# Kernel tuning notes

Measured on AMD Instinct MI355X. Metric: run time of the kernel, lower is better.

The kernel has to match this reference:

```python
import jax, jax.numpy as jnp
import numpy as np

D_MODEL = 1024
N_HEADS = 16
N_KV = 4
HEAD_DIM = D_MODEL // N_HEADS  # 64
SEQ = 2048
BATCH = 2
CAP = 50.0
EPS = 1e-5
THETA = 10000.0


def setup_inputs() -> dict:
    key = jax.random.key(0)
    ks = jax.random.split(key, 5)
    s = 0.02  # keep pre-attention logits in a sane range
    return {
        'x':   jax.random.normal(ks[0], (BATCH, SEQ, D_MODEL), dtype=jnp.float32),
        'w_q': jax.random.normal(ks[1], (D_MODEL, N_HEADS * HEAD_DIM), dtype=jnp.float32) * s,
        'w_k': jax.random.normal(ks[2], (D_MODEL, N_KV * HEAD_DIM), dtype=jnp.float32) * s,
        'w_v': jax.random.normal(ks[3], (D_MODEL, N_KV * HEAD_DIM), dtype=jnp.float32) * s,
        'w_o': jax.random.normal(ks[4], (N_HEADS * HEAD_DIM, D_MODEL), dtype=jnp.float32) * s,
    }


def _rms_norm(x, eps=EPS):
    return x * jax.lax.rsqrt(jnp.mean(jnp.square(x), axis=-1, keepdims=True) + eps)


def _rope_cos_sin(seq_len, head_dim, theta=THETA):
    inv_freq = 1.0 / (theta ** (jnp.arange(0, head_dim, 2, dtype=jnp.float32) / head_dim))
    freqs = jnp.arange(seq_len, dtype=jnp.float32)[:, None] * inv_freq[None, :]  # (S, d/2)
    return jnp.cos(freqs)[None, :, None, :], jnp.sin(freqs)[None, :, None, :]  # (1,S,1,d/2)


def _apply_rope(x, cos, sin):
    d = x.shape[-1] // 2
    x1, x2 = x[..., :d], x[..., d:]
    return jnp.concatenate([x1 * cos - x2 * sin, x2 * cos + x1 * sin], axis=-1).astype(x.dtype)


def reference(x, w_q, w_k, w_v, w_o):
    B, S, _ = x.shape
    q = (x @ w_q).reshape(B, S, N_HEADS, HEAD_DIM)
    k = (x @ w_k).reshape(B, S, N_KV, HEAD_DIM)
    v = (x @ w_v).reshape(B, S, N_KV, HEAD_DIM)

    # QK RMS-norm (no learned scale)
    q = _rms_norm(q)
    k = _rms_norm(k)

    cos, sin = _rope_cos_sin(S, HEAD_DIM)
    q = _apply_rope(q, cos, sin)
    k = _apply_rope(k, cos, sin)

    # GQA: repeat kv heads to match query heads
    rep = N_HEADS // N_KV
    k = jnp.repeat(k, rep, axis=2)
    v = jnp.repeat(v, rep, axis=2)

    scores = jnp.einsum('bqhd,bkhd->bhqk', q, k) / np.sqrt(HEAD_DIM).astype(np.float32)
    # softcap in float32, as in the original
    scores = jnp.tanh(scores.astype(jnp.float32) / CAP) * CAP
    causal = jnp.tril(jnp.ones((S, S), dtype=bool))  # (S, S)
    scores = jnp.where(causal[None, None], scores, -jnp.inf)
    probs = jax.nn.softmax(scores, axis=-1)  # dropout=0.0 -> identity

    y = jnp.einsum('bhqk,bkhd->bqhd', probs, v).reshape(B, S, N_HEADS * HEAD_DIM)
    return y @ w_o
```

## Files before the change

kernel.cpp:

```cpp
#include <hip/hip_runtime.h>
#include <hip/hip_bf16.h>
#include <math.h>

#define D_MODEL 1024
#define N_HEADS 16
#define N_KV 4
#define HEAD_DIM 64
#define SEQ 2048
#define BATCH 2
#define M_TOK (BATCH * SEQ)

typedef unsigned int u32;
typedef unsigned short u16;
typedef __attribute__((ext_vector_type(8))) short short8;
typedef __attribute__((ext_vector_type(4))) float f32x4;
typedef __attribute__((ext_vector_type(16))) float f32x16;
typedef __attribute__((ext_vector_type(2))) float f32x2;

#define AS1 __attribute__((address_space(1)))
#define AS3 __attribute__((address_space(3)))

__device__ __forceinline__ u16 f2bf(float f) {
  union { __hip_bfloat16 h; u16 u; } c; c.h = __float2bfloat16(f); return c.u;
}
__device__ __forceinline__ float bf2f(u16 v) {
  union { u32 u; float f; } c; c.u = (u32)v << 16; return c.f;
}
__device__ __forceinline__ u32 cvtpk(float lo, float hi) {
  u32 r; asm("v_cvt_pk_bf16_f32 %0, %1, %2" : "=v"(r) : "v"(lo), "v"(hi)); return r;
}
__device__ __forceinline__ void plswap(u32& a, u32& b) {
  asm volatile("v_permlane32_swap_b32 %0, %1" : "+v"(a), "+v"(b));
}
__device__ __forceinline__ float exp2fast(float x) { return __builtin_amdgcn_exp2f(x); }
__device__ __forceinline__ float rcpfast(float x) { return __builtin_amdgcn_rcpf(x); }
__device__ __forceinline__ f32x2 pk_mul(f32x2 a, f32x2 b) {
  f32x2 d; asm("v_pk_mul_f32 %0, %1, %2" : "=v"(d) : "v"(a), "v"(b)); return d;
}
__device__ __forceinline__ f32x2 pk_fma(f32x2 a, f32x2 b, f32x2 c) {
  f32x2 d; asm("v_pk_fma_f32 %0, %1, %2, %3" : "=v"(d) : "v"(a), "v"(b), "v"(c)); return d;
}

__global__ __launch_bounds__(256) void prep_kernel(const float* __restrict__ x,
                                                   const float* __restrict__ wq,
                                                   const float* __restrict__ wk,
                                                   const float* __restrict__ wv,
                                                   const float* __restrict__ wo,
                                                   u16* __restrict__ xb,
                                                   u16* __restrict__ wT,
                                                   u16* __restrict__ woT) {
  int bx = blockIdx.x;
  if (bx < 512) {
    const size_t base = (size_t)bx * 8192;
#pragma unroll
    for (int j = 0; j < 4; ++j) {
      size_t e = base + j * 2048 + threadIdx.x * 8;
      float4 f0 = *(const float4*)(x + e);
      float4 f1 = *(const float4*)(x + e + 4);
      uint4 u;
      u.x = cvtpk(f0.x, f0.y); u.y = cvtpk(f0.z, f0.w);
      u.z = cvtpk(f1.x, f1.y); u.w = cvtpk(f1.z, f1.w);
      *(uint4*)(xb + e) = u;
    }
    return;
  }
  bx -= 512;
  __shared__ float t[32][33];
  const float* src; u16* dst; int N, ntm, nts;
  if (bx < 1024)      { src = wq; dst = wT;                 N = 1024; ntm = 31; nts = 5; }
  else if (bx < 1280) { bx -= 1024; src = wk; dst = wT + (1024 << 10); N = 256; ntm = 7; nts = 3; }
  else if (bx < 1536) { bx -= 1280; src = wv; dst = wT + (1280 << 10); N = 256; ntm = 7; nts = 3; }
  else                { bx -= 1536; src = wo; dst = woT;    N = 1024; ntm = 31; nts = 5; }
  const int n0 = (bx & ntm) << 5, k0 = (bx >> nts) << 5;
  const int xx = threadIdx.x & 31, y = threadIdx.x >> 5;
#pragma unroll
  for (int i = 0; i < 4; ++i) {
    int r = y + (i << 3);
    t[r][xx] = src[(size_t)(k0 + r) * N + n0 + xx];
  }
  __syncthreads();
#pragma unroll
  for (int i = 0; i < 4; ++i) {
    int r = y + (i << 3);
    dst[(size_t)(n0 + r) * 1024 + k0 + xx] = f2bf(t[xx][r]);
  }
}

__global__ __launch_bounds__(256, 2) void qkvgemm_kernel(const u16* __restrict__ xb,
                                                         const u16* __restrict__ wT,
                                                         u16* __restrict__ Qbf,
                                                         u16* __restrict__ Kbf,
                                                         u16* __restrict__ Vt) {
  __shared__ uint4 SM[4][512];
  const int tid = threadIdx.x;
  const int w = tid >> 6, l = tid & 63;
  const int wr = w >> 1, wc = w & 1;
  int wg = ((int)blockIdx.x & 7) * 48 + ((int)blockIdx.x >> 3);
  const int mt = wg / 12, nb = wg - mt * 12;
  const int m0 = mt << 7;

  f32x4 acc[4][4];
#pragma unroll
  for (int m = 0; m < 4; ++m)
#pragma unroll
    for (int n = 0; n < 4; ++n)
#pragma unroll
      for (int j = 0; j < 4; ++j) acc[m][n][j] = 0.f;

  auto stage = [&](int buf, int k0) {
    const u16* Ab = xb + (size_t)m0 * 1024 + k0;
#pragma unroll
    for (int r = 0; r < 2; ++r) {
      int i = (w << 1) + r;
      int row = (i << 4) + (l >> 2);
      const u16* g = Ab + (size_t)row * 1024 + ((l & 3) << 3);
      __builtin_amdgcn_global_load_lds((const AS1 void*)g,
          (AS3 void*)((char*)SM + (buf << 13) + (i << 10)), 16, 0, 0);
    }
    const u16* Bb = wT + (size_t)(nb << 7) * 1024 + k0;
#pragma unroll
    for (int r = 0; r < 2; ++r) {
      int i = (w << 1) + r;
      int row = (i << 4) + (l >> 2);
      const u16* g = Bb + (size_t)row * 1024 + ((l & 3) << 3);
      __builtin_amdgcn_global_load_lds((const AS1 void*)g,
          (AS3 void*)((char*)SM + ((2 + buf) << 13) + (i << 10)), 16, 0, 0);
    }
  };

  stage(0, 0);
#pragma unroll 1
  for (int kt = 0; kt < 32; ++kt) {
    __syncthreads();
    if (kt + 1 < 32) stage((kt + 1) & 1, (kt + 1) << 5);
    const char* Ab = (const char*)SM + ((kt & 1) << 13);
    const char* Bb = (const char*)SM + ((2 + (kt & 1)) << 13);
    short8 af[4], bf[4];
#pragma unroll
    for (int m = 0; m < 4; ++m)
      af[m] = *(const short8*)(Ab + ((wr * 64 + m * 16 + (l & 15)) << 6) + ((l >> 4) << 4));
#pragma unroll
    for (int n = 0; n < 4; ++n)
      bf[n] = *(const short8*)(Bb + ((wc * 64 + n * 16 + (l & 15)) << 6) + ((l >> 4) << 4));
#pragma unroll
    for (int m = 0; m < 4; ++m)
#pragma unroll
      for (int n = 0; n < 4; ++n)
        acc[m][n] = __builtin_amdgcn_mfma_f32_16x16x32_bf16(af[m], bf[n], acc[m][n], 0, 0, 0);
  }

  __syncthreads();
  const int b = m0 >> 11;
  const int pos0 = (m0 & 2047) + wr * 64;
  const int lg = l >> 4, lc = l & 15;
  u16* lds = (u16*)((char*)SM + (w << 13));

  if (nb < 10) {
    float rs[4][4];
#pragma unroll
    for (int m = 0; m < 4; ++m)
#pragma unroll
      for (int j = 0; j < 4; ++j) {
        float ssq = 0.f;
#pragma unroll
        for (int n = 0; n < 4; ++n) ssq = fmaf(acc[m][n][j], acc[m][n][j], ssq);
        ssq += __shfl_xor(ssq, 1); ssq += __shfl_xor(ssq, 2);
        ssq += __shfl_xor(ssq, 4); ssq += __shfl_xor(ssq, 8);
        rs[m][j] = rsqrtf(ssq * (1.f / 64.f) + 1e-5f);
      }
    const float osc = (nb < 8) ? 0.0025f : 1.0f;
    const float invf0 = powf(10000.0f, (float)lc * (-1.f / 32.f));
    const float invf1 = powf(10000.0f, (float)(lc + 16) * (-1.f / 32.f));
#pragma unroll
    for (int m = 0; m < 4; ++m) {
#pragma unroll
      for (int j = 0; j < 4; ++j) {
        const int row = m * 16 + lg * 4 + j;
        const float pos = (float)(pos0 + row);
        float s0, c0, s1, c1;
        sincosf(pos * invf0, &s0, &c0);
        sincosf(pos * invf1, &s1, &c1);
        const float r_ = rs[m][j];
        float x0 = acc[m][0][j] * r_, x1 = acc[m][1][j] * r_;
        float x2 = acc[m][2][j] * r_, x3 = acc[m][3][j] * r_;
        u16 o0 = f2bf((x0 * c0 - x2 * s0) * osc);
        u16 o1 = f2bf((x1 * c1 - x3 * s1) * osc);
        u16 o2 = f2bf((x2 * c0 + x0 * s0) * osc);
        u16 o3 = f2bf((x3 * c1 + x1 * s1) * osc);
        const int rb = row << 6, xr = (row & 7) << 3;
        lds[rb + (lc ^ xr)] = o0;
        lds[rb + ((16 + lc) ^ xr)] = o1;
        lds[rb + ((32 + lc) ^ xr)] = o2;
        lds[rb + ((48 + lc) ^ xr)] = o3;
      }
    }
  } else {
#pragma unroll
    for (int m = 0; m < 4; ++m)
#pragma unroll
      for (int n = 0; n < 4; ++n) {
        const int d = n * 16 + lc;
        const int tok = m * 16 + lg * 4;
        uint2 u;
        u.x = cvtpk(acc[m][n][0], acc[m][n][1]);
        u.y = cvtpk(acc[m][n][2], acc[m][n][3]);
        *(uint2*)(lds + (d << 6) + (tok ^ ((d & 7) << 3))) = u;
      }
  }
  __syncthreads();

  u16* gp; int rstride;
  if (nb < 8)       { gp = Qbf + ((size_t)((b * 16 + nb * 2 + wc) * 2048 + pos0) << 6); rstride = 64; }
  else if (nb < 10) { gp = Kbf + ((size_t)((b * 4 + (nb - 8) * 2 + wc) * 2048 + pos0) << 6); rstride = 64; }
  else              { gp = Vt + (((size_t)((b * 4 + (nb - 10) * 2 + wc) * 64)) << 11) + pos0; rstride = 2048; }
#pragma unroll
  for (int ic = 0; ic < 8; ++ic) {
    const int c = (ic << 6) + l;
    const int row = c >> 3, col8 = (c & 7) << 3;
    uint4 v = *(const uint4*)(lds + (row << 6) + (col8 ^ ((row & 7) << 3)));
    *(uint4*)(gp + (size_t)row * rstride + col8) = v;
  }
}

__global__ __launch_bounds__(256, 2) void gemm_kernel(const u16* __restrict__ A,
                                                      const u16* __restrict__ BT,
                                                      float* __restrict__ C) {
  __shared__ uint4 SM[4][512];
  const int tid = threadIdx.x;
  const int w = tid >> 6, l = tid & 63;
  const int wr = w >> 1, wc = w & 1;
  int wg = ((int)blockIdx.x & 7) * 32 + ((int)blockIdx.x >> 3);
  const int m0 = (wg >> 3) << 7, n0 = (wg & 7) << 7;

  f32x4 acc[4][4];
#pragma unroll
  for (int m = 0; m < 4; ++m)
#pragma unroll
    for (int n = 0; n < 4; ++n)
#pragma unroll
      for (int j = 0; j < 4; ++j) acc[m][n][j] = 0.f;

  auto stage = [&](int buf, int k0) {
    const u16* Ab = A + (size_t)m0 * 1024 + k0;
#pragma unroll
    for (int r = 0; r < 2; ++r) {
      int i = (w << 1) + r;
      int row = (i << 4) + (l >> 2);
      const u16* g = Ab + (size_t)row * 1024 + ((l & 3) << 3);
      __builtin_amdgcn_global_load_lds((const AS1 void*)g,
          (AS3 void*)((char*)SM + (buf << 13) + (i << 10)), 16, 0, 0);
    }
    const u16* Bb = BT + (size_t)n0 * 1024 + k0;
#pragma unroll
    for (int r = 0; r < 2; ++r) {
      int i = (w << 1) + r;
      int row = (i << 4) + (l >> 2);
      const u16* g = Bb + (size_t)row * 1024 + ((l & 3) << 3);
      __builtin_amdgcn_global_load_lds((const AS1 void*)g,
          (AS3 void*)((char*)SM + ((2 + buf) << 13) + (i << 10)), 16, 0, 0);
    }
  };

  stage(0, 0);
#pragma unroll 1
  for (int kt = 0; kt < 32; ++kt) {
    __syncthreads();
    if (kt + 1 < 32) stage((kt + 1) & 1, (kt + 1) << 5);
    const char* Ab = (const char*)SM + ((kt & 1) << 13);
    const char* Bb = (const char*)SM + ((2 + (kt & 1)) << 13);
    short8 af[4], bf[4];
#pragma unroll
    for (int m = 0; m < 4; ++m)
      af[m] = *(const short8*)(Ab + ((wr * 64 + m * 16 + (l & 15)) << 6) + ((l >> 4) << 4));
#pragma unroll
    for (int n = 0; n < 4; ++n)
      bf[n] = *(const short8*)(Bb + ((wc * 64 + n * 16 + (l & 15)) << 6) + ((l >> 4) << 4));
#pragma unroll
    for (int m = 0; m < 4; ++m)
#pragma unroll
      for (int n = 0; n < 4; ++n)
        acc[m][n] = __builtin_amdgcn_mfma_f32_16x16x32_bf16(af[m], bf[n], acc[m][n], 0, 0, 0);
  }

#pragma unroll
  for (int m = 0; m < 4; ++m) {
    int row0 = m0 + wr * 64 + m * 16 + ((l >> 4) << 2);
#pragma unroll
    for (int n = 0; n < 4; ++n) {
      int col = n0 + wc * 64 + n * 16 + (l & 15);
#pragma unroll
      for (int j = 0; j < 4; ++j)
        C[(size_t)(row0 + j) * 1024 + col] = acc[m][n][j];
    }
  }
}

__global__ __launch_bounds__(256) void combine_kernel(const u16* __restrict__ P0,
                                                      const u16* __restrict__ P1,
                                                      const float* __restrict__ L0,
                                                      const float* __restrict__ L1,
                                                      u16* __restrict__ ybf) {
  const int hrow = (blockIdx.x << 1) + (threadIdx.x >> 7);
  const int chunk = threadIdx.x & 127;
  const int h = chunk >> 3;
  const int b = hrow >> 10, posl = hrow & 1023;
  const size_t tok = (size_t)(b * 2048 + 1024 + posl);
  const float rl = rcpfast(L0[hrow * 16 + h] + L1[hrow * 16 + h]);
  uint4 a = *(const uint4*)(P0 + ((size_t)hrow << 10) + (chunk << 3));
  uint4 c = *(const uint4*)(P1 + ((size_t)hrow << 10) + (chunk << 3));
  uint4 o;
#pragma unroll
  for (int e = 0; e < 4; ++e) {
    u32 ua = ((const u32*)&a)[e], uc = ((const u32*)&c)[e];
    float v0 = (bf2f((u16)(ua & 0xffff)) + bf2f((u16)(uc & 0xffff))) * rl;
    float v1 = (bf2f((u16)(ua >> 16)) + bf2f((u16)(uc >> 16))) * rl;
    ((u32*)&o)[e] = cvtpk(v0, v1);
  }
  *(uint4*)(ybf + tok * 1024 + (chunk << 3)) = o;
}

__device__ __forceinline__ short8 rdfrag(const uint4* lds, int row, int cb) {
  int byte = ((row << 7) + cb) ^ ((row & 7) << 4);
  return *(const short8*)((const char*)lds + byte);
}

__global__ __launch_bounds__(256, 3) void attn_kernel(const u16* __restrict__ Qbf,
                                                      const u16* __restrict__ Kbf,
                                                      const u16* __restrict__ Vt,
                                                      u16* __restrict__ ybf,
                                                      u16* __restrict__ P0,
                                                      u16* __restrict__ P1,
                                                      float* __restrict__ L0,
                                                      float* __restrict__ L1) {
  __shared__ uint4 KV[4][512];
  const int tid = threadIdx.x;
  const int g = blockIdx.x & 7;
  const int u = blockIdx.x >> 3;
  int j, kt0, kt1; bool diagEnd;
  if (u < 32)      { j = u;       kt0 = 0;  kt1 = (j >> 1) + 1; diagEnd = true; }
  else if (u < 64) { j = u;       kt0 = 0;  kt1 = 16;           diagEnd = false; }
  else             { j = 127 - u; kt0 = 16; kt1 = (j >> 1) + 1; diagEnd = true; }
  const bool slot1 = (u >= 64);

  const int b = g >> 2, hkv = g & 3;
  const int w = tid >> 6, l = tid & 63;
  const int ql = l & 31, myh = l >> 5;
  const int h = hkv * 4 + w;
  const int q0 = j << 5;
  const int qg = q0 + ql;

  const u16* Kg = Kbf + (((size_t)g) << 11) * 64;
  const u16* Vg = Vt + (((size_t)g) << 6) * 2048;

  short8 bq[4];
  {
    const u16* Qg = Qbf + ((size_t)((b * 16 + h) * 2048 + qg)) * 64 + myh * 8;
    bq[0] = *(const short8*)(Qg);
    bq[1] = *(const short8*)(Qg + 16);
    bq[2] = *(const short8*)(Qg + 32);
    bq[3] = *(const short8*)(Qg + 48);
  }

  f32x16 o0, o1;
#pragma unroll
  for (int i = 0; i < 16; ++i) { o0[i] = 0.f; o1[i] = 0.f; }
  float l_run = 0.f;

  auto stage = [&](int buf, int kt) {
    const u16* gk = Kg + ((size_t)(kt << 6)) * 64;
    const u16* gv = Vg + (kt << 6);
#pragma unroll
    for (int i = 0; i < 2; ++i) {
      int c = tid + (i << 8);
      int row = c >> 3, off = c & 7;
      uint4 kk4 = *(const uint4*)(gk + row * 64 + (off << 3));
      uint4 vv4 = *(const uint4*)(gv + (size_t)row * 2048 + (off << 3));
      int byte = ((row << 7) + (off << 4)) ^ ((row & 7) << 4);
      *(uint4*)((char*)KV[buf << 1] + byte) = kk4;
      *(uint4*)((char*)KV[(buf << 1) + 1] + byte) = vv4;
    }
  };

  stage(0, kt0);

  const float PC2 = -0.33333333f;
  const float SC1 = 72.13475204444817f;
  const float SC0 = -11.541560327111708f;
  const f32x2 PC2v = {PC2, PC2};
  const f32x2 SC1v = {SC1, SC1};
  const f32x2 SC0v = {SC0, SC0};
  const f32x2 ONEv = {1.0f, 1.0f};

#pragma unroll 1
  for (int kt = kt0; kt < kt1; ++kt) {
    const int buf = kt & 1;
    __syncthreads();
    if (kt + 1 < kt1) stage(buf ^ 1, kt + 1);
    const bool last = diagEnd && (kt == kt1 - 1);
    const bool havehi = !last || (j & 1);
    const uint4* Kl = KV[buf << 1];
    const uint4* Vl = KV[(buf << 1) + 1];

    f32x16 s0, s1;
#pragma unroll
    for (int i = 0; i < 16; ++i) { s0[i] = 0.f; s1[i] = 0.f; }
    __builtin_amdgcn_s_setprio(1);
#pragma unroll
    for (int c = 0; c < 4; ++c) {
      short8 ak = rdfrag(Kl, ql, (c << 5) + (myh << 4));
      s0 = __builtin_amdgcn_mfma_f32_32x32x16_bf16(ak, bq[c], s0, 0, 0, 0);
    }
    if (havehi) {
#pragma unroll
      for (int c = 0; c < 4; ++c) {
        short8 ak = rdfrag(Kl, 32 + ql, (c << 5) + (myh << 4));
        s1 = __builtin_amdgcn_mfma_f32_32x32x16_bf16(ak, bq[c], s1, 0, 0, 0);
      }
    }
    __builtin_amdgcn_s_setprio(0);

    float lsum = 0.f;
    auto cap_full = [&](f32x16& s) {
#pragma unroll
      for (int p = 0; p < 8; ++p) {
        f32x2 z; z.x = s[2 * p]; z.y = s[2 * p + 1];
        f32x2 z2 = pk_mul(z, z);
        f32x2 zc = pk_fma(z2, PC2v, ONEv);
        f32x2 zs = pk_mul(z, SC1v);
        f32x2 ar = pk_fma(zs, zc, SC0v);
        float p0 = exp2fast(ar.x);
        float p1 = exp2fast(ar.y);
        s[2 * p] = p0; s[2 * p + 1] = p1;
        lsum += p0; lsum += p1;
      }
    };
    auto cap_diag = [&](f32x16& s) {
#pragma unroll
      for (int i = 0; i < 16; ++i) {
        int kl = (i & 3) + ((i >> 2) << 3) + (myh << 2);
        float z = s[i];
        float zc = fmaf(z * z, PC2, 1.0f);
        float p = exp2fast(fmaf(z * zc, SC1, SC0));
        p = (kl <= ql) ? p : 0.f;
        s[i] = p; lsum += p;
      }
    };
    if (!last)       { cap_full(s0); cap_full(s1); }
    else if (j & 1)  { cap_full(s0); cap_diag(s1); }
    else             { cap_diag(s0); }
    l_run += lsum;

    short8 pa[4];
    auto mkpa = [&](const f32x16& P, int c0) {
#pragma unroll
      for (int ci = 0; ci < 2; ++ci) {
        const int rb = ci << 3;
        u32 A = cvtpk(P[rb + 0], P[rb + 1]);
        u32 Cw = cvtpk(P[rb + 2], P[rb + 3]);
        u32 B = cvtpk(P[rb + 4], P[rb + 5]);
        u32 D = cvtpk(P[rb + 6], P[rb + 7]);
        plswap(A, B); plswap(Cw, D);
        union { u32 u[4]; short8 s; } pw_;
        pw_.u[0] = A; pw_.u[1] = Cw; pw_.u[2] = B; pw_.u[3] = D;
        pa[c0 + ci] = pw_.s;
      }
    };
    mkpa(s0, 0);
    if (havehi) mkpa(s1, 2);

    __builtin_amdgcn_s_setprio(1);
#pragma unroll
    for (int c = 0; c < 2; ++c) {
      short8 av = rdfrag(Vl, ql, (c << 5) + (myh << 4));
      o0 = __builtin_amdgcn_mfma_f32_32x32x16_bf16(av, pa[c], o0, 0, 0, 0);
      short8 av1 = rdfrag(Vl, 32 + ql, (c << 5) + (myh << 4));
      o1 = __builtin_amdgcn_mfma_f32_32x32x16_bf16(av1, pa[c], o1, 0, 0, 0);
    }
    if (havehi) {
#pragma unroll
      for (int c = 2; c < 4; ++c) {
        short8 av = rdfrag(Vl, ql, (c << 5) + (myh << 4));
        o0 = __builtin_amdgcn_mfma_f32_32x32x16_bf16(av, pa[c], o0, 0, 0, 0);
        short8 av1 = rdfrag(Vl, 32 + ql, (c << 5) + (myh << 4));
        o1 = __builtin_amdgcn_mfma_f32_32x32x16_bf16(av1, pa[c], o1, 0, 0, 0);
      }
    }
    __builtin_amdgcn_s_setprio(0);
  }

  float lr = l_run + __shfl_xor(l_run, 32);
  if (u < 32) {
    float rl = rcpfast(lr);
    u16* yr = ybf + ((size_t)(b * 2048 + qg)) * 1024 + h * 64;
#pragma unroll
    for (int i = 0; i < 16; i += 2) {
      int dof = (i & 3) + ((i >> 2) << 3) + (myh << 2);
      *(u32*)(yr + dof) = cvtpk(o0[i] * rl, o0[i + 1] * rl);
      *(u32*)(yr + 32 + dof) = cvtpk(o1[i] * rl, o1[i + 1] * rl);
    }
  } else {
    const size_t hrow = (size_t)(b * 1024 + qg - 1024);
    u16* Ob = slot1 ? P1 : P0;
    float* Lb = slot1 ? L1 : L0;
    u16* yr = Ob + (hrow << 10) + h * 64;
#pragma unroll
    for (int i = 0; i < 16; i += 2) {
      int dof = (i & 3) + ((i >> 2) << 3) + (myh << 2);
      *(u32*)(yr + dof) = cvtpk(o0[i], o0[i + 1]);
      *(u32*)(yr + 32 + dof) = cvtpk(o1[i], o1[i + 1]);
    }
    if (l < 32) Lb[hrow * 16 + h] = lr;
  }
}

extern "C" void kernel_launch(void* const* d_in, const int* in_sizes, int n_in,
                              void* d_out, int out_size, void* d_ws, size_t ws_size,
                              hipStream_t stream) {
  (void)in_sizes; (void)n_in; (void)out_size; (void)ws_size;
  const float* x  = (const float*)d_in[0];
  const float* wq = (const float*)d_in[1];
  const float* wk = (const float*)d_in[2];
  const float* wv = (const float*)d_in[3];
  const float* wo = (const float*)d_in[4];
  float* out = (float*)d_out;

  char* ws = (char*)d_ws;
  u16* xb  = (u16*)ws;
  u16* ybf = (u16*)(ws + (8u << 20));
  u16* woT = (u16*)(ws + (16u << 20));
  u16* wT  = (u16*)(ws + (18u << 20));
  u16* Qbf = (u16*)(ws + (21u << 20));
  u16* Kbf = (u16*)(ws + (29u << 20));
  u16* Vt  = (u16*)(ws + (31u << 20));
  u16* P0  = (u16*)(ws + (33u << 20));
  u16* P1  = (u16*)(ws + (37u << 20));
  float* L0 = (float*)(ws + (41u << 20));
  float* L1 = (float*)(ws + (41u << 20) + (128u << 10));

  prep_kernel<<<dim3(3072), 256, 0, stream>>>(x, wq, wk, wv, wo, xb, wT, woT);
  qkvgemm_kernel<<<dim3(384), 256, 0, stream>>>(xb, wT, Qbf, Kbf, Vt);
  attn_kernel<<<dim3(768), 256, 0, stream>>>(Qbf, Kbf, Vt, ybf, P0, P1, L0, L1);
  combine_kernel<<<dim3(1024), 256, 0, stream>>>(P0, P1, L0, L1, ybf);
  gemm_kernel<<<dim3(256), 256, 0, stream>>>(ybf, woT, out);
}
```

Baseline: 94.66 us.

## Halve GEMM M-tile to 64 rows to double workgroup count and occupancy

Both the fused QKV projection GEMM and the output projection GEMM now use 64x128 tiles instead of 128x128. This doubles the grid (768 and 512 workgroups) to fill more of the MI355X's compute units, and it lowers accumulator registers and LDS so more workgroups can be resident per CU (QKV launch bounds go to 3). The QKV epilogue is reworked for the smaller tile, including a new LDS transpose layout for the V output. The cost is less reuse of B-tile loads per MFMA and more total global traffic for the weights.

```diff
diff --git a/kernel.cpp b/kernel.cpp
--- a/kernel.cpp
+++ b/kernel.cpp
@@ -86,45 +86,41 @@
   }
 }
 
-__global__ __launch_bounds__(256, 2) void qkvgemm_kernel(const u16* __restrict__ xb,
+__global__ __launch_bounds__(256, 3) void qkvgemm_kernel(const u16* __restrict__ xb,
                                                          const u16* __restrict__ wT,
                                                          u16* __restrict__ Qbf,
                                                          u16* __restrict__ Kbf,
                                                          u16* __restrict__ Vt) {
-  __shared__ uint4 SM[4][512];
+  __shared__ uint4 SMA[2][256];
+  __shared__ uint4 SMB[2][512];
   const int tid = threadIdx.x;
   const int w = tid >> 6, l = tid & 63;
   const int wr = w >> 1, wc = w & 1;
-  int wg = ((int)blockIdx.x & 7) * 48 + ((int)blockIdx.x >> 3);
+  int wg = ((int)blockIdx.x & 7) * 96 + ((int)blockIdx.x >> 3);
   const int mt = wg / 12, nb = wg - mt * 12;
-  const int m0 = mt << 7;
-
-  f32x4 acc[4][4];
-#pragma unroll
-  for (int m = 0; m < 4; ++m)
+  const int m0 = mt << 6;
+
+  f32x4 acc[2][4];
+#pragma unroll
+  for (int m = 0; m < 2; ++m)
 #pragma unroll
     for (int n = 0; n < 4; ++n)
 #pragma unroll
       for (int j = 0; j < 4; ++j) acc[m][n][j] = 0.f;
 
   auto stage = [&](int buf, int k0) {
-    const u16* Ab = xb + (size_t)m0 * 1024 + k0;
+    {
+      const u16* g = xb + (size_t)(m0 + (w << 4) + (l >> 2)) * 1024 + k0 + ((l & 3) << 3);
+      __builtin_amdgcn_global_load_lds((const AS1 void*)g,
+          (AS3 void*)((char*)SMA[buf] + (w << 10)), 16, 0, 0);
+    }
+    const u16* Bb = wT + (size_t)(nb << 7) * 1024 + k0;
 #pragma unroll
     for (int r = 0; r < 2; ++r) {
       int i = (w << 1) + r;
-      int row = (i << 4) + (l >> 2);
-      const u16* g = Ab + (size_t)row * 1024 + ((l & 3) << 3);
+      const u16* g = Bb + (size_t)((i << 4) + (l >> 2)) * 1024 + ((l & 3) << 3);
       __builtin_amdgcn_global_load_lds((const AS1 void*)g,
-          (AS3 void*)((char*)SM + (buf << 13) + (i << 10)), 16, 0, 0);
-    }
-    const u16* Bb = wT + (size_t)(nb << 7) * 1024 + k0;
-#pragma unroll
-    for (int r = 0; r < 2; ++r) {
-      int i = (w << 1) + r;
-      int row = (i << 4) + (l >> 2);
-      const u16* g = Bb + (size_t)row * 1024 + ((l & 3) << 3);
-      __builtin_amdgcn_global_load_lds((const AS1 void*)g,
-          (AS3 void*)((char*)SM + ((2 + buf) << 13) + (i << 10)), 16, 0, 0);
+          (AS3 void*)((char*)SMB[buf] + (i << 10)), 16, 0, 0);
     }
   };
 
@@ -133,17 +129,17 @@
   for (int kt = 0; kt < 32; ++kt) {
     __syncthreads();
     if (kt + 1 < 32) stage((kt + 1) & 1, (kt + 1) << 5);
-    const char* Ab = (const char*)SM + ((kt & 1) << 13);
-    const char* Bb = (const char*)SM + ((2 + (kt & 1)) << 13);
-    short8 af[4], bf[4];
-#pragma unroll
-    for (int m = 0; m < 4; ++m)
-      af[m] = *(const short8*)(Ab + ((wr * 64 + m * 16 + (l & 15)) << 6) + ((l >> 4) << 4));
+    const char* Ab = (const char*)SMA[kt & 1];
+    const char* Bb = (const char*)SMB[kt & 1];
+    short8 af[2], bf[4];
+#pragma unroll
+    for (int m = 0; m < 2; ++m)
+      af[m] = *(const short8*)(Ab + (((wr << 5) + m * 16 + (l & 15)) << 6) + ((l >> 4) << 4));
 #pragma unroll
     for (int n = 0; n < 4; ++n)
-      bf[n] = *(const short8*)(Bb + ((wc * 64 + n * 16 + (l & 15)) << 6) + ((l >> 4) << 4));
-#pragma unroll
-    for (int m = 0; m < 4; ++m)
+      bf[n] = *(const short8*)(Bb + (((wc << 6) + n * 16 + (l & 15)) << 6) + ((l >> 4) << 4));
+#pragma unroll
+    for (int m = 0; m < 2; ++m)
 #pragma unroll
       for (int n = 0; n < 4; ++n)
         acc[m][n] = __builtin_amdgcn_mfma_f32_16x16x32_bf16(af[m], bf[n], acc[m][n], 0, 0, 0);
@@ -151,14 +147,14 @@
 
   __syncthreads();
   const int b = m0 >> 11;
-  const int pos0 = (m0 & 2047) + wr * 64;
+  const int pos0 = (m0 & 2047) + (wr << 5);
   const int lg = l >> 4, lc = l & 15;
-  u16* lds = (u16*)((char*)SM + (w << 13));
+  u16* lds = (u16*)((char*)SMB + (w << 12));
 
   if (nb < 10) {
-    float rs[4][4];
-#pragma unroll
-    for (int m = 0; m < 4; ++m)
+    float rs[2][4];
+#pragma unroll
+    for (int m = 0; m < 2; ++m)
 #pragma unroll
       for (int j = 0; j < 4; ++j) {
         float ssq = 0.f;
@@ -172,10 +168,10 @@
     const float invf0 = powf(10000.0f, (float)lc * (-1.f / 32.f));
     const float invf1 = powf(10000.0f, (float)(lc + 16) * (-1.f / 32.f));
 #pragma unroll
-    for (int m = 0; m < 4; ++m) {
+    for (int m = 0; m < 2; ++m) {
 #pragma unroll
       for (int j = 0; j < 4; ++j) {
-        const int row = m * 16 + lg * 4 + j;
+        const int row = m * 16 + (lg << 2) + j;
         const float pos = (float)(pos0 + row);
         float s0, c0, s1, c1;
         sincosf(pos * invf0, &s0, &c0);
@@ -194,70 +190,73 @@
         lds[rb + ((48 + lc) ^ xr)] = o3;
       }
     }
+    __syncthreads();
+    u16* gp;
+    if (nb < 8) gp = Qbf + ((size_t)((b * 16 + nb * 2 + wc) * 2048 + pos0) << 6);
+    else        gp = Kbf + ((size_t)((b * 4 + (nb - 8) * 2 + wc) * 2048 + pos0) << 6);
+#pragma unroll
+    for (int ic = 0; ic < 4; ++ic) {
+      const int c = (ic << 6) + l;
+      const int row = c >> 3, col8 = (c & 7) << 3;
+      uint4 v = *(const uint4*)(lds + (row << 6) + (col8 ^ ((row & 7) << 3)));
+      *(uint4*)(gp + (size_t)row * 64 + col8) = v;
+    }
   } else {
 #pragma unroll
-    for (int m = 0; m < 4; ++m)
+    for (int m = 0; m < 2; ++m)
 #pragma unroll
       for (int n = 0; n < 4; ++n) {
         const int d = n * 16 + lc;
-        const int tok = m * 16 + lg * 4;
+        const int tok = m * 16 + (lg << 2);
         uint2 u;
         u.x = cvtpk(acc[m][n][0], acc[m][n][1]);
         u.y = cvtpk(acc[m][n][2], acc[m][n][3]);
-        *(uint2*)(lds + (d << 6) + (tok ^ ((d & 7) << 3))) = u;
-      }
-  }
-  __syncthreads();
-
-  u16* gp; int rstride;
-  if (nb < 8)       { gp = Qbf + ((size_t)((b * 16 + nb * 2 + wc) * 2048 + pos0) << 6); rstride = 64; }
-  else if (nb < 10) { gp = Kbf + ((size_t)((b * 4 + (nb - 8) * 2 + wc) * 2048 + pos0) << 6); rstride = 64; }
-  else              { gp = Vt + (((size_t)((b * 4 + (nb - 10) * 2 + wc) * 64)) << 11) + pos0; rstride = 2048; }
-#pragma unroll
-  for (int ic = 0; ic < 8; ++ic) {
-    const int c = (ic << 6) + l;
-    const int row = c >> 3, col8 = (c & 7) << 3;
-    uint4 v = *(const uint4*)(lds + (row << 6) + (col8 ^ ((row & 7) << 3)));
-    *(uint4*)(gp + (size_t)row * rstride + col8) = v;
+        *(uint2*)(lds + (d << 5) + (tok ^ ((d & 3) << 3))) = u;
+      }
+    __syncthreads();
+    u16* gp = Vt + (((size_t)((b * 4 + (nb - 10) * 2 + wc) * 64)) << 11) + pos0;
+#pragma unroll
+    for (int ic = 0; ic < 4; ++ic) {
+      const int c = (ic << 6) + l;
+      const int d = c >> 2, col8 = (c & 3) << 3;
+      uint4 v = *(const uint4*)(lds + (d << 5) + (col8 ^ ((d & 3) << 3)));
+      *(uint4*)(gp + (size_t)d * 2048 + col8) = v;
+    }
   }
 }
 
 __global__ __launch_bounds__(256, 2) void gemm_kernel(const u16* __restrict__ A,
                                                       const u16* __restrict__ BT,
                                                       float* __restrict__ C) {
-  __shared__ uint4 SM[4][512];
+  __shared__ uint4 SMA[2][256];
+  __shared__ uint4 SMB[2][512];
   const int tid = threadIdx.x;
   const int w = tid >> 6, l = tid & 63;
   const int wr = w >> 1, wc = w & 1;
-  int wg = ((int)blockIdx.x & 7) * 32 + ((int)blockIdx.x >> 3);
-  const int m0 = (wg >> 3) << 7, n0 = (wg & 7) << 7;
-
-  f32x4 acc[4][4];
-#pragma unroll
-  for (int m = 0; m < 4; ++m)
+  int wg = ((int)blockIdx.x & 7) * 64 + ((int)blockIdx.x >> 3);
+  const int m0 = (wg >> 3) << 6, n0 = (wg & 7) << 7;
+
+  f32x4 acc[2][4];
+#pragma unroll
+  for (int m = 0; m < 2; ++m)
 #pragma unroll
     for (int n = 0; n < 4; ++n)
 #pragma unroll
       for (int j = 0; j < 4; ++j) acc[m][n][j] = 0.f;
 
   auto stage = [&](int buf, int k0) {
-    const u16* Ab = A + (size_t)m0 * 1024 + k0;
+    {
+      const u16* g = A + (size_t)(m0 + (w << 4) + (l >> 2)) * 1024 + k0 + ((l & 3) << 3);
+      __builtin_amdgcn_global_load_lds((const AS1 void*)g,
+          (AS3 void*)((char*)SMA[buf] + (w << 10)), 16, 0, 0);
+    }
+    const u16* Bb = BT + (size_t)n0 * 1024 + k0;
 #pragma unroll
     for (int r = 0; r < 2; ++r) {
       int i = (w << 1) + r;
-      int row = (i << 4) + (l >> 2);
-      const u16* g = Ab + (size_t)row * 1024 + ((l & 3) << 3);
+      const u16* g = Bb + (size_t)((i << 4) + (l >> 2)) * 1024 + ((l & 3) << 3);
       __builtin_amdgcn_global_load_lds((const AS1 void*)g,
-          (AS3 void*)((char*)SM + (buf << 13) + (i << 10)), 16, 0, 0);
-    }
-    const u16* Bb = BT + (size_t)n0 * 1024 + k0;
-#pragma unroll
-    for (int r = 0; r < 2; ++r) {
-      int i = (w << 1) + r;
-      int row = (i << 4) + (l >> 2);
-      const u16* g = Bb + (size_t)row * 1024 + ((l & 3) << 3);
-      __builtin_amdgcn_global_load_lds((const AS1 void*)g,
-          (AS3 void*)((char*)SM + ((2 + buf) << 13) + (i << 10)), 16, 0, 0);
+          (AS3 void*)((char*)SMB[buf] + (i << 10)), 16, 0, 0);
     }
   };
 
@@ -266,28 +265,28 @@
   for (int kt = 0; kt < 32; ++kt) {
     __syncthreads();
     if (kt + 1 < 32) stage((kt + 1) & 1, (kt + 1) << 5);
-    const char* Ab = (const char*)SM + ((kt & 1) << 13);
-    const char* Bb = (const char*)SM + ((2 + (kt & 1)) << 13);
-    short8 af[4], bf[4];
-#pragma unroll
-    for (int m = 0; m < 4; ++m)
-      af[m] = *(const short8*)(Ab + ((wr * 64 + m * 16 + (l & 15)) << 6) + ((l >> 4) << 4));
+    const char* Ab = (const char*)SMA[kt & 1];
+    const char* Bb = (const char*)SMB[kt & 1];
+    short8 af[2], bf[4];
+#pragma unroll
+    for (int m = 0; m < 2; ++m)
+      af[m] = *(const short8*)(Ab + (((wr << 5) + m * 16 + (l & 15)) << 6) + ((l >> 4) << 4));
 #pragma unroll
     for (int n = 0; n < 4; ++n)
-      bf[n] = *(const short8*)(Bb + ((wc * 64 + n * 16 + (l & 15)) << 6) + ((l >> 4) << 4));
-#pragma unroll
-    for (int m = 0; m < 4; ++m)
+      bf[n] = *(const short8*)(Bb + (((wc << 6) + n * 16 + (l & 15)) << 6) + ((l >> 4) << 4));
+#pragma unroll
+    for (int m = 0; m < 2; ++m)
 #pragma unroll
       for (int n = 0; n < 4; ++n)
         acc[m][n] = __builtin_amdgcn_mfma_f32_16x16x32_bf16(af[m], bf[n], acc[m][n], 0, 0, 0);
   }
 
 #pragma unroll
-  for (int m = 0; m < 4; ++m) {
-    int row0 = m0 + wr * 64 + m * 16 + ((l >> 4) << 2);
+  for (int m = 0; m < 2; ++m) {
+    int row0 = m0 + (wr << 5) + m * 16 + ((l >> 4) << 2);
 #pragma unroll
     for (int n = 0; n < 4; ++n) {
-      int col = n0 + wc * 64 + n * 16 + (l & 15);
+      int col = n0 + (wc << 6) + n * 16 + (l & 15);
 #pragma unroll
       for (int j = 0; j < 4; ++j)
         C[(size_t)(row0 + j) * 1024 + col] = acc[m][n][j];
@@ -538,8 +537,8 @@
   float* L1 = (float*)(ws + (41u << 20) + (128u << 10));
 
   prep_kernel<<<dim3(3072), 256, 0, stream>>>(x, wq, wk, wv, wo, xb, wT, woT);
-  qkvgemm_kernel<<<dim3(384), 256, 0, stream>>>(xb, wT, Qbf, Kbf, Vt);
+  qkvgemm_kernel<<<dim3(768), 256, 0, stream>>>(xb, wT, Qbf, Kbf, Vt);
   attn_kernel<<<dim3(768), 256, 0, stream>>>(Qbf, Kbf, Vt, ybf, P0, P1, L0, L1);
   combine_kernel<<<dim3(1024), 256, 0, stream>>>(P0, P1, L0, L1, ybf);
-  gemm_kernel<<<dim3(256), 256, 0, stream>>>(ybf, woT, out);
-}
+  gemm_kernel<<<dim3(512), 256, 0, stream>>>(ybf, woT, out);
+}
```

Result: slower. 96.58 us (+2.0%).

## Fuse split-KV combine into attention via atomic last-block merge

Applied to the files above, without the earlier changes.

Drops the separate combine kernel. Each split attention block bumps an atomic counter per (group, query tile) after writing its partial output and row sum. The second block to finish merges both partials and writes the normalized bf16 output directly. This saves one kernel launch and its extra pass over memory, at the cost of threadfences, an atomic and a serialized tail in some attention blocks. The counters are zeroed in the prep kernel.

```diff
diff --git a/kernel.cpp b/kernel.cpp
--- a/kernel.cpp
+++ b/kernel.cpp
@@ -48,8 +48,10 @@
                                                    const float* __restrict__ wo,
                                                    u16* __restrict__ xb,
                                                    u16* __restrict__ wT,
-                                                   u16* __restrict__ woT) {
+                                                   u16* __restrict__ woT,
+                                                   u32* __restrict__ cnt) {
   int bx = blockIdx.x;
+  if (bx == 0) cnt[threadIdx.x] = 0;
   if (bx < 512) {
     const size_t base = (size_t)bx * 8192;
 #pragma unroll
@@ -295,30 +297,6 @@
   }
 }
 
-__global__ __launch_bounds__(256) void combine_kernel(const u16* __restrict__ P0,
-                                                      const u16* __restrict__ P1,
-                                                      const float* __restrict__ L0,
-                                                      const float* __restrict__ L1,
-                                                      u16* __restrict__ ybf) {
-  const int hrow = (blockIdx.x << 1) + (threadIdx.x >> 7);
-  const int chunk = threadIdx.x & 127;
-  const int h = chunk >> 3;
-  const int b = hrow >> 10, posl = hrow & 1023;
-  const size_t tok = (size_t)(b * 2048 + 1024 + posl);
-  const float rl = rcpfast(L0[hrow * 16 + h] + L1[hrow * 16 + h]);
-  uint4 a = *(const uint4*)(P0 + ((size_t)hrow << 10) + (chunk << 3));
-  uint4 c = *(const uint4*)(P1 + ((size_t)hrow << 10) + (chunk << 3));
-  uint4 o;
-#pragma unroll
-  for (int e = 0; e < 4; ++e) {
-    u32 ua = ((const u32*)&a)[e], uc = ((const u32*)&c)[e];
-    float v0 = (bf2f((u16)(ua & 0xffff)) + bf2f((u16)(uc & 0xffff))) * rl;
-    float v1 = (bf2f((u16)(ua >> 16)) + bf2f((u16)(uc >> 16))) * rl;
-    ((u32*)&o)[e] = cvtpk(v0, v1);
-  }
-  *(uint4*)(ybf + tok * 1024 + (chunk << 3)) = o;
-}
-
 __device__ __forceinline__ short8 rdfrag(const uint4* lds, int row, int cb) {
   int byte = ((row << 7) + cb) ^ ((row & 7) << 4);
   return *(const short8*)((const char*)lds + byte);
@@ -331,8 +309,10 @@
                                                       u16* __restrict__ P0,
                                                       u16* __restrict__ P1,
                                                       float* __restrict__ L0,
-                                                      float* __restrict__ L1) {
+                                                      float* __restrict__ L1,
+                                                      u32* __restrict__ cnt) {
   __shared__ uint4 KV[4][512];
+  __shared__ u32 oldsh;
   const int tid = threadIdx.x;
   const int g = blockIdx.x & 7;
   const int u = blockIdx.x >> 3;
@@ -510,6 +490,39 @@
       *(u32*)(yr + 32 + dof) = cvtpk(o1[i], o1[i + 1]);
     }
     if (l < 32) Lb[hrow * 16 + h] = lr;
+
+    __threadfence();
+    __syncthreads();
+    if (tid == 0)
+      oldsh = __hip_atomic_fetch_add(&cnt[(g << 5) + (j - 32)], 1u,
+                                     __ATOMIC_ACQ_REL, __HIP_MEMORY_SCOPE_AGENT);
+    __syncthreads();
+    if (oldsh == 1) {
+      __threadfence();
+      const int rowbase0 = b * 1024 + (q0 - 1024);
+#pragma unroll
+      for (int it = 0; it < 4; ++it) {
+        int idx = tid + (it << 8);
+        int r = idx >> 5;
+        int c8 = (idx & 31) << 3;
+        int hl = c8 >> 6;
+        size_t hr = (size_t)(rowbase0 + r);
+        float rl2 = rcpfast(L0[hr * 16 + (hkv << 2) + hl] +
+                            L1[hr * 16 + (hkv << 2) + hl]);
+        uint4 a = *(const uint4*)(P0 + (hr << 10) + (hkv << 8) + c8);
+        uint4 c = *(const uint4*)(P1 + (hr << 10) + (hkv << 8) + c8);
+        uint4 o;
+#pragma unroll
+        for (int e = 0; e < 4; ++e) {
+          u32 ua = ((const u32*)&a)[e], uc = ((const u32*)&c)[e];
+          float v0 = (bf2f((u16)(ua & 0xffff)) + bf2f((u16)(uc & 0xffff))) * rl2;
+          float v1 = (bf2f((u16)(ua >> 16)) + bf2f((u16)(uc >> 16))) * rl2;
+          ((u32*)&o)[e] = cvtpk(v0, v1);
+        }
+        size_t tok = (size_t)(b * 2048 + q0 + r);
+        *(uint4*)(ybf + (tok << 10) + (hkv << 8) + c8) = o;
+      }
+    }
   }
 }
 
@@ -536,10 +549,10 @@
   u16* P1  = (u16*)(ws + (37u << 20));
   float* L0 = (float*)(ws + (41u << 20));
   float* L1 = (float*)(ws + (41u << 20) + (128u << 10));
-
-  prep_kernel<<<dim3(3072), 256, 0, stream>>>(x, wq, wk, wv, wo, xb, wT, woT);
+  u32* cnt  = (u32*)(ws + (41u << 20) + (256u << 10));
+
+  prep_kernel<<<dim3(3072), 256, 0, stream>>>(x, wq, wk, wv, wo, xb, wT, woT, cnt);
   qkvgemm_kernel<<<dim3(384), 256, 0, stream>>>(xb, wT, Qbf, Kbf, Vt);
-  attn_kernel<<<dim3(768), 256, 0, stream>>>(Qbf, Kbf, Vt, ybf, P0, P1, L0, L1);
-  combine_kernel<<<dim3(1024), 256, 0, stream>>>(P0, P1, L0, L1, ybf);
+  attn_kernel<<<dim3(768), 256, 0, stream>>>(Qbf, Kbf, Vt, ybf, P0, P1, L0, L1, cnt);
   gemm_kernel<<<dim3(256), 256, 0, stream>>>(ybf, woT, out);
 }
```

Result: slower. 193.4 us (+104.3%).
